# Kernel optimization log

Hardware: AMD Instinct MI355X
Metric: run time of the kernel (lower is better)

Reference implementation:

```python
import jax, jax.numpy as jnp
import numpy as np

E = 8192   # line-graph nodes (edges of g)
N = 4096   # graph nodes
FIN = 64   # in_feats
FOUT = 64  # out_feats
H = FOUT // 2
BN_EPS = 1e-5


def _linear_params(k, fan_in):
    kw, kb = jax.random.split(k)
    s = 1.0 / np.sqrt(fan_in)
    w = jax.random.uniform(kw, (H, fan_in), jnp.float32, -s, s)
    b = jax.random.uniform(kb, (H,), jnp.float32, -s, s)
    return w, b


def setup_inputs() -> dict:
    key = jax.random.key(0)
    ks = jax.random.split(key, 12)
    inp = {}
    inp["y"] = jax.random.normal(ks[0], (E, FIN), jnp.float32)
    inp["deg_g"] = jax.random.uniform(ks[1], (N,), jnp.float32)  # unused in forward
    inp["g_a1"] = jnp.zeros((N, N), jnp.float32)                  # unused in forward
    # adjacency-like 0/1 matrices, sparse pattern stored dense (as th.mm expects)
    inp["lg_a1"] = (jax.random.uniform(ks[2], (E, E)) < (8.0 / E)).astype(jnp.float32)
    inp["pm"] = (jax.random.uniform(ks[3], (N, E)) < (2.0 / N)).astype(jnp.float32)
    inp["pd"] = (jax.random.uniform(ks[4], (N, E)) < (2.0 / N)).astype(jnp.float32)
    inp["theta_y_w"], inp["theta_y_b"] = _linear_params(ks[5], FIN)
    inp["theta_y_r_w"], inp["theta_y_r_b"] = _linear_params(ks[6], FIN)
    inp["gamma_a_w"], inp["gamma_a_b"] = _linear_params(ks[7], FIN)
    inp["gamma_x_w"], inp["gamma_x_b"] = _linear_params(ks[8], FOUT)
    inp["gamma_a_r_w"], inp["gamma_a_r_b"] = _linear_params(ks[9], FIN)
    inp["gamma_x_r_w"], inp["gamma_x_r_b"] = _linear_params(ks[10], FOUT)
    inp["bn_x_w"] = jnp.ones((FOUT,), jnp.float32)
    inp["bn_x_b"] = jnp.zeros((FOUT,), jnp.float32)
    inp["bn_y_w"] = jnp.ones((FOUT,), jnp.float32)
    inp["bn_y_b"] = jnp.zeros((FOUT,), jnp.float32)
    return inp


def _bn(x, w, b):
    # BatchNorm2d on [B, C, 1, 1] in training mode == per-channel batch norm
    # with biased variance over the row (batch) dimension.
    m = x.mean(0)
    v = jnp.mean((x - m) ** 2, axis=0)
    return (x - m) * jax.lax.rsqrt(v + BN_EPS) * w + b


def reference(y, deg_g, g_a1, lg_a1, pm, pd,
              theta_y_w, theta_y_b, theta_y_r_w, theta_y_r_b,
              gamma_a_w, gamma_a_b, gamma_x_w, gamma_x_b,
              gamma_a_r_w, gamma_a_r_b, gamma_x_r_w, gamma_x_r_b,
              bn_x_w, bn_x_b, bn_y_w, bn_y_b):
    pd_y = pd @ y                                        # [N, FIN]
    x_r = pd_y @ theta_y_r_w.T + theta_y_r_b             # [N, H]
    x = pd_y @ theta_y_w.T + theta_y_b                   # [N, H]
    x = jnp.concatenate([x, jax.nn.relu(x_r)], axis=1)   # [N, FOUT]
    x = _bn(x, bn_x_w, bn_x_b)
    pm_x = pm.T @ x                                      # [E, FOUT]
    lg_y = lg_a1 @ y                                     # [E, FIN] (computed once; torch computes it twice, same math)
    y_r = (lg_y @ gamma_a_r_w.T + gamma_a_r_b) + (pm_x @ gamma_x_r_w.T + gamma_x_r_b)
    y_n = (lg_y @ gamma_a_w.T + gamma_a_b) + (pm_x @ gamma_x_w.T + gamma_x_b)
    y_out = jnp.concatenate([y_n, jax.nn.relu(y_r)], axis=1)  # [E, FOUT]
    return _bn(y_out, bn_y_w, bn_y_b)
```

## Files before the change

kernel.cpp:

```cpp
#include <hip/hip_runtime.h>

typedef unsigned int uint_t;
typedef unsigned short ushort_t;
typedef unsigned long long ull_t;
typedef uint_t nvec4 __attribute__((ext_vector_type(4)));

#define SLOTS 48

__device__ __forceinline__ float bcast(float v, int k) {
    union { float f; int i; } x; x.f = v;
    int r = __builtin_amdgcn_readlane(x.i, k);
    union { int i; float f; } y2; y2.i = r;
    return y2.f;
}

__global__ __launch_bounds__(256) void stream_gather_kernel(
    const float* __restrict__ lg, const float* __restrict__ pd,
    const float* __restrict__ pm, const float* __restrict__ y,
    float* __restrict__ lg_y, float* __restrict__ pd_y,
    ushort_t* __restrict__ pm_keys, uint_t* __restrict__ pm_counts)
{
    __shared__ ushort_t sIdx[4][SLOTS];
    const int lane = threadIdx.x & 63;
    const int wv = threadIdx.x >> 6;
    const int wid = blockIdx.x * 4 + wv;
    const float* A;
    int row;
    if (wid < 8192)       { row = wid;         A = lg; }
    else if (wid < 12288) { row = wid - 8192;  A = pd; }
    else                  { row = wid - 12288; A = pm; }

    const nvec4* ap = (const nvec4*)(A + (size_t)row * 8192);
    ushort_t* slice = sIdx[wv];
    const ull_t lt = (1ull << lane) - 1ull;

    nvec4 buf[16];
    #pragma unroll
    for (int i = 0; i < 16; ++i)
        buf[i] = __builtin_nontemporal_load(ap + i * 64 + lane);

    uint_t cnt = 0;
    #pragma unroll
    for (int pp = 0; pp < 32; pp += 16) {
        #pragma unroll
        for (int i = 0; i < 16; ++i) {
            nvec4 c = buf[i];
            if (pp == 0)
                buf[i] = __builtin_nontemporal_load(ap + (16 + i) * 64 + lane);
            uint_t a0 = c.x, a1 = c.y, a2 = c.z, a3 = c.w;
            ull_t m = __ballot((a0 | a1 | a2 | a3) != 0u);
            if (m) {
                ull_t m0 = __ballot(a0 != 0u);
                ull_t m1 = __ballot(a1 != 0u);
                ull_t m2 = __ballot(a2 != 0u);
                ull_t m3 = __ballot(a3 != 0u);
                uint_t c0 = (uint_t)__popcll(m0), c1 = (uint_t)__popcll(m1);
                uint_t c2 = (uint_t)__popcll(m2);
                uint_t o0 = cnt + (uint_t)__popcll(m0 & lt);
                uint_t o1 = cnt + c0 + (uint_t)__popcll(m1 & lt);
                uint_t o2 = cnt + c0 + c1 + (uint_t)__popcll(m2 & lt);
                uint_t o3 = cnt + c0 + c1 + c2 + (uint_t)__popcll(m3 & lt);
                int j = (pp + i) * 256 + lane * 4;
                if (a0 && o0 < SLOTS) slice[o0] = (ushort_t)(j + 0);
                if (a1 && o1 < SLOTS) slice[o1] = (ushort_t)(j + 1);
                if (a2 && o2 < SLOTS) slice[o2] = (ushort_t)(j + 2);
                if (a3 && o3 < SLOTS) slice[o3] = (ushort_t)(j + 3);
                cnt += (uint_t)(__popcll(m0) + __popcll(m1) +
                                __popcll(m2) + __popcll(m3));
            }
        }
    }
    if (cnt > SLOTS) cnt = SLOTS;

    if (wid >= 12288) {
        if (lane == 0) pm_counts[row] = cnt;
        if (lane < (int)cnt) pm_keys[(size_t)row * SLOTS + lane] = slice[lane];
        return;
    }
    float a0 = 0.f, a1 = 0.f, a2 = 0.f, a3 = 0.f;
    uint_t i = 0;
    for (; i + 4 <= cnt; i += 4) {
        int j0 = slice[i + 0], j1 = slice[i + 1];
        int j2 = slice[i + 2], j3 = slice[i + 3];
        a0 += y[(size_t)j0 * 64 + lane];
        a1 += y[(size_t)j1 * 64 + lane];
        a2 += y[(size_t)j2 * 64 + lane];
        a3 += y[(size_t)j3 * 64 + lane];
    }
    for (; i < cnt; ++i) a0 += y[(size_t)slice[i] * 64 + lane];
    float acc = (a0 + a1) + (a2 + a3);
    if (wid < 8192) lg_y[(size_t)row * 64 + lane] = acc;
    else            pd_y[(size_t)row * 64 + lane] = acc;
}

__global__ __launch_bounds__(256) void xlin_kernel(
    const float* __restrict__ pd_y,
    const float* __restrict__ wt, const float* __restrict__ bt,
    const float* __restrict__ wr, const float* __restrict__ br,
    float* __restrict__ x_raw, float* __restrict__ stats_x)
{
    __shared__ float red[2][4][64];
    const int wave = threadIdx.x >> 6, lane = threadIdx.x & 63;
    const float* wsrc = (lane < 32) ? (wt + lane * 64) : (wr + (lane - 32) * 64);
    float wreg[64];
    const float4* wp = (const float4*)wsrc;
    #pragma unroll
    for (int q = 0; q < 16; ++q) {
        float4 t = wp[q];
        wreg[q * 4 + 0] = t.x; wreg[q * 4 + 1] = t.y;
        wreg[q * 4 + 2] = t.z; wreg[q * 4 + 3] = t.w;
    }
    float bias = (lane < 32) ? bt[lane] : br[lane - 32];
    float s1 = 0.f, s2 = 0.f;
    const int row0 = (blockIdx.x * 4 + wave) * 8;
    for (int r = 0; r < 8; ++r) {
        int row = row0 + r;
        float xv = pd_y[(size_t)row * 64 + lane];
        float acc = bias;
        #pragma unroll
        for (int k = 0; k < 64; ++k) acc = fmaf(bcast(xv, k), wreg[k], acc);
        if (lane >= 32) acc = fmaxf(acc, 0.f);
        x_raw[(size_t)row * 64 + lane] = acc;
        s1 += acc; s2 += acc * acc;
    }
    red[0][wave][lane] = s1; red[1][wave][lane] = s2;
    __syncthreads();
    if (wave == 0) {
        float a = 0.f, b = 0.f;
        #pragma unroll
        for (int w = 0; w < 4; ++w) { a += red[0][w][lane]; b += red[1][w][lane]; }
        atomicAdd(&stats_x[lane], a);
        atomicAdd(&stats_x[64 + lane], b);
    }
}

__global__ __launch_bounds__(256) void scatter_kernel(
    const ushort_t* __restrict__ pm_keys, const uint_t* __restrict__ pm_counts,
    const float* __restrict__ x_raw, const float* __restrict__ stats_x,
    const float* __restrict__ bnxw, const float* __restrict__ bnxb,
    float* __restrict__ pm_x)
{
    const int lane = threadIdx.x & 63;
    const int row = blockIdx.x * 4 + (threadIdx.x >> 6);
    float mean = stats_x[lane] * (1.f / 4096.f);
    float var  = fmaxf(stats_x[64 + lane] * (1.f / 4096.f) - mean * mean, 0.f);
    float rstd = rsqrtf(var + 1e-5f);
    float scale = rstd * bnxw[lane];
    float shift = bnxb[lane] - mean * scale;
    const ushort_t* slice = pm_keys + (size_t)row * SLOTS;
    uint_t cnt = pm_counts[row];
    float xb = fmaf(x_raw[(size_t)row * 64 + lane], scale, shift);
    for (uint_t i = 0; i < cnt; ++i) {
        int e = slice[i];
        atomicAdd(&pm_x[(size_t)e * 64 + lane], xb);
    }
}

__global__ __launch_bounds__(256) void ylin_kernel(
    const float* __restrict__ lg_y, const float* __restrict__ pm_x,
    const float* __restrict__ wa, const float* __restrict__ ba,
    const float* __restrict__ wx, const float* __restrict__ bx,
    const float* __restrict__ war, const float* __restrict__ bar,
    const float* __restrict__ wxr, const float* __restrict__ bxr,
    float* __restrict__ yraw, float* __restrict__ stats_y)
{
    __shared__ float red[2][4][64];
    const int wave = threadIdx.x >> 6, lane = threadIdx.x & 63;
    const float* s1p = (lane < 32) ? (wa + lane * 64) : (war + (lane - 32) * 64);
    const float* s2p = (lane < 32) ? (wx + lane * 64) : (wxr + (lane - 32) * 64);
    float w1[64], w2[64];
    {
        const float4* p1 = (const float4*)s1p;
        const float4* p2 = (const float4*)s2p;
        #pragma unroll
        for (int q = 0; q < 16; ++q) {
            float4 t1 = p1[q], t2 = p2[q];
            w1[q * 4 + 0] = t1.x; w1[q * 4 + 1] = t1.y;
            w1[q * 4 + 2] = t1.z; w1[q * 4 + 3] = t1.w;
            w2[q * 4 + 0] = t2.x; w2[q * 4 + 1] = t2.y;
            w2[q * 4 + 2] = t2.z; w2[q * 4 + 3] = t2.w;
        }
    }
    float bias = (lane < 32) ? (ba[lane] + bx[lane])
                             : (bar[lane - 32] + bxr[lane - 32]);
    float s1 = 0.f, s2 = 0.f;
    const int row0 = (blockIdx.x * 4 + wave) * 8;
    for (int r = 0; r < 8; ++r) {
        int row = row0 + r;
        float lv = lg_y[(size_t)row * 64 + lane];
        float pv = pm_x[(size_t)row * 64 + lane];
        float acc = bias;
        #pragma unroll
        for (int k = 0; k < 64; ++k) {
            acc = fmaf(bcast(lv, k), w1[k], acc);
            acc = fmaf(bcast(pv, k), w2[k], acc);
        }
        if (lane >= 32) acc = fmaxf(acc, 0.f);
        yraw[(size_t)row * 64 + lane] = acc;
        s1 += acc; s2 += acc * acc;
    }
    red[0][wave][lane] = s1; red[1][wave][lane] = s2;
    __syncthreads();
    if (wave == 0) {
        float a = 0.f, b = 0.f;
        #pragma unroll
        for (int w = 0; w < 4; ++w) { a += red[0][w][lane]; b += red[1][w][lane]; }
        atomicAdd(&stats_y[lane], a);
        atomicAdd(&stats_y[64 + lane], b);
    }
}

__global__ __launch_bounds__(256) void bny_kernel(
    float* __restrict__ yraw, const float* __restrict__ stats_y,
    const float* __restrict__ bnyw, const float* __restrict__ bnyb)
{
    int idx = blockIdx.x * 256 + threadIdx.x;
    int c = idx & 63;
    float mean = stats_y[c] * (1.f / 8192.f);
    float var  = fmaxf(stats_y[64 + c] * (1.f / 8192.f) - mean * mean, 0.f);
    float rstd = rsqrtf(var + 1e-5f);
    yraw[idx] = (yraw[idx] - mean) * rstd * bnyw[c] + bnyb[c];
}

extern "C" void kernel_launch(void* const* d_in, const int* in_sizes, int n_in,
                              void* d_out, int out_size, void* d_ws, size_t ws_size,
                              hipStream_t stream)
{
    const float* y     = (const float*)d_in[0];
    const float* lg_a1 = (const float*)d_in[3];
    const float* pm    = (const float*)d_in[4];
    const float* pd    = (const float*)d_in[5];
    const float* th_w  = (const float*)d_in[6];
    const float* th_b  = (const float*)d_in[7];
    const float* thr_w = (const float*)d_in[8];
    const float* thr_b = (const float*)d_in[9];
    const float* ga_w  = (const float*)d_in[10];
    const float* ga_b  = (const float*)d_in[11];
    const float* gx_w  = (const float*)d_in[12];
    const float* gx_b  = (const float*)d_in[13];
    const float* gar_w = (const float*)d_in[14];
    const float* gar_b = (const float*)d_in[15];
    const float* gxr_w = (const float*)d_in[16];
    const float* gxr_b = (const float*)d_in[17];
    const float* bnx_w = (const float*)d_in[18];
    const float* bnx_b = (const float*)d_in[19];
    const float* bny_w = (const float*)d_in[20];
    const float* bny_b = (const float*)d_in[21];

    char* ws = (char*)d_ws;
    float* stats_x = (float*)ws;
    float* stats_y = (float*)(ws + 1024);
    float* pm_x    = (float*)(ws + 2048);
    const size_t zero_bytes = 2048 + (size_t)8192 * 64 * 4;
    float* pd_y  = (float*)(ws + zero_bytes);
    float* lg_y  = pd_y + (size_t)4096 * 64;
    float* x_raw = lg_y + (size_t)8192 * 64;
    ushort_t* pm_keys = (ushort_t*)(x_raw + (size_t)4096 * 64);
    uint_t* pm_counts = (uint_t*)(pm_keys + (size_t)4096 * SLOTS);
    float* yraw  = (float*)d_out;

    (void)hipMemsetAsync(d_ws, 0, zero_bytes, stream);

    stream_gather_kernel<<<4096, 256, 0, stream>>>(lg_a1, pd, pm, y,
                                                   lg_y, pd_y,
                                                   pm_keys, pm_counts);
    xlin_kernel<<<128, 256, 0, stream>>>(pd_y, th_w, th_b, thr_w, thr_b,
                                         x_raw, stats_x);
    scatter_kernel<<<1024, 256, 0, stream>>>(pm_keys, pm_counts, x_raw, stats_x,
                                             bnx_w, bnx_b, pm_x);
    ylin_kernel<<<256, 256, 0, stream>>>(lg_y, pm_x, ga_w, ga_b, gx_w, gx_b,
                                         gar_w, gar_b, gxr_w, gxr_b,
                                         yraw, stats_y);
    bny_kernel<<<2048, 256, 0, stream>>>(yraw, stats_y, bny_w, bny_b);
}
```

Baseline: 574.5 us.

## Split dense streaming into a chunk-interleaved bitmask pass plus separate gather

```diff
diff --git a/kernel.cpp b/kernel.cpp
--- a/kernel.cpp
+++ b/kernel.cpp
@@ -6,6 +6,12 @@
 typedef uint_t nvec4 __attribute__((ext_vector_type(4)));
 
 #define SLOTS 48
+
+#define LG_CHUNK_END 262144
+#define PD_CHUNK_END 393216
+#define TOT_CHUNKS   524288
+#define STREAM_WAVES 8192
+#define CHUNK_ITERS  (TOT_CHUNKS / STREAM_WAVES)
 
 __device__ __forceinline__ float bcast(float v, int k) {
     union { float f; int i; } x; x.f = v;
@@ -14,9 +20,51 @@
     return y2.f;
 }
 
-__global__ __launch_bounds__(256) void stream_gather_kernel(
+__device__ __forceinline__ const nvec4* chunk_ptr(int c, const float* lg,
+                                                  const float* pd, const float* pm) {
+    if (c < LG_CHUNK_END) return (const nvec4*)(lg + (size_t)c * 256);
+    if (c < PD_CHUNK_END) return (const nvec4*)(pd + (size_t)(c - LG_CHUNK_END) * 256);
+    return (const nvec4*)(pm + (size_t)(c - PD_CHUNK_END) * 256);
+}
+
+__global__ __launch_bounds__(256) void mask_stream_kernel(
     const float* __restrict__ lg, const float* __restrict__ pd,
-    const float* __restrict__ pm, const float* __restrict__ y,
+    const float* __restrict__ pm, ull_t* __restrict__ maskbuf)
+{
+    const int lane = threadIdx.x & 63;
+    const int w = blockIdx.x * 4 + (threadIdx.x >> 6);
+
+    #pragma unroll
+    for (int g = 0; g < CHUNK_ITERS / 4; ++g) {
+        nvec4 b[4];
+        #pragma unroll
+        for (int k = 0; k < 4; ++k) {
+            int c = (g * 4 + k) * STREAM_WAVES + w;
+            b[k] = __builtin_nontemporal_load(chunk_ptr(c, lg, pd, pm) + lane);
+        }
+        #pragma unroll
+        for (int k = 0; k < 4; ++k) {
+            int c = (g * 4 + k) * STREAM_WAVES + w;
+            nvec4 v = b[k];
+            ull_t m0 = 0, m1 = 0, m2 = 0, m3 = 0;
+            ull_t any = __ballot((v.x | v.y | v.z | v.w) != 0u);
+            if (any) {
+                m0 = __ballot(v.x != 0u);
+                m1 = __ballot(v.y != 0u);
+                m2 = __ballot(v.z != 0u);
+                m3 = __ballot(v.w != 0u);
+            }
+            if (lane < 4) {
+                ull_t out = (lane & 2) ? ((lane & 1) ? m3 : m2)
+                                       : ((lane & 1) ? m1 : m0);
+                maskbuf[(size_t)c * 4 + lane] = out;
+            }
+        }
+    }
+}
+
+__global__ __launch_bounds__(256) void gather2_kernel(
+    const ull_t* __restrict__ maskbuf, const float* __restrict__ y,
     float* __restrict__ lg_y, float* __restrict__ pd_y,
     ushort_t* __restrict__ pm_keys, uint_t* __restrict__ pm_counts)
 {
@@ -24,55 +72,52 @@
     const int lane = threadIdx.x & 63;
     const int wv = threadIdx.x >> 6;
     const int wid = blockIdx.x * 4 + wv;
-    const float* A;
-    int row;
-    if (wid < 8192)       { row = wid;         A = lg; }
-    else if (wid < 12288) { row = wid - 8192;  A = pd; }
-    else                  { row = wid - 12288; A = pm; }
-
-    const nvec4* ap = (const nvec4*)(A + (size_t)row * 8192);
+    int row, kind;
+    size_t cbase;
+    if (wid < 8192)       { row = wid;         kind = 0; cbase = (size_t)row * 32; }
+    else if (wid < 12288) { row = wid - 8192;  kind = 1; cbase = LG_CHUNK_END + (size_t)row * 32; }
+    else                  { row = wid - 12288; kind = 2; cbase = PD_CHUNK_END + (size_t)row * 32; }
+
+    const ulonglong2* mp = (const ulonglong2*)(maskbuf + cbase * 4);
+    ulonglong2 t = mp[lane];
+    ull_t u0 = t.x, u1 = t.y;
+    uint_t c = (uint_t)(__popcll(u0) + __popcll(u1));
+
+    uint_t inc = c;
+    #pragma unroll
+    for (int d = 1; d < 64; d <<= 1) {
+        uint_t tt = __shfl_up(inc, d, 64);
+        if (lane >= d) inc += tt;
+    }
+    uint_t off = inc - c;
+    uint_t tot = __shfl(inc, 63, 64);
+
     ushort_t* slice = sIdx[wv];
-    const ull_t lt = (1ull << lane) - 1ull;
-
-    nvec4 buf[16];
-    #pragma unroll
-    for (int i = 0; i < 16; ++i)
-        buf[i] = __builtin_nontemporal_load(ap + i * 64 + lane);
-
-    uint_t cnt = 0;
-    #pragma unroll
-    for (int pp = 0; pp < 32; pp += 16) {
-        #pragma unroll
-        for (int i = 0; i < 16; ++i) {
-            nvec4 c = buf[i];
-            if (pp == 0)
-                buf[i] = __builtin_nontemporal_load(ap + (16 + i) * 64 + lane);
-            uint_t a0 = c.x, a1 = c.y, a2 = c.z, a3 = c.w;
-            ull_t m = __ballot((a0 | a1 | a2 | a3) != 0u);
-            if (m) {
-                ull_t m0 = __ballot(a0 != 0u);
-                ull_t m1 = __ballot(a1 != 0u);
-                ull_t m2 = __ballot(a2 != 0u);
-                ull_t m3 = __ballot(a3 != 0u);
-                uint_t c0 = (uint_t)__popcll(m0), c1 = (uint_t)__popcll(m1);
-                uint_t c2 = (uint_t)__popcll(m2);
-                uint_t o0 = cnt + (uint_t)__popcll(m0 & lt);
-                uint_t o1 = cnt + c0 + (uint_t)__popcll(m1 & lt);
-                uint_t o2 = cnt + c0 + c1 + (uint_t)__popcll(m2 & lt);
-                uint_t o3 = cnt + c0 + c1 + c2 + (uint_t)__popcll(m3 & lt);
-                int j = (pp + i) * 256 + lane * 4;
-                if (a0 && o0 < SLOTS) slice[o0] = (ushort_t)(j + 0);
-                if (a1 && o1 < SLOTS) slice[o1] = (ushort_t)(j + 1);
-                if (a2 && o2 < SLOTS) slice[o2] = (ushort_t)(j + 2);
-                if (a3 && o3 < SLOTS) slice[o3] = (ushort_t)(j + 3);
-                cnt += (uint_t)(__popcll(m0) + __popcll(m1) +
-                                __popcll(m2) + __popcll(m3));
-            }
-        }
-    }
-    if (cnt > SLOTS) cnt = SLOTS;
-
-    if (wid >= 12288) {
+    {
+        int ui = 2 * lane;
+        int basecol = (ui >> 2) * 256 + (ui & 3);
+        ull_t u = u0;
+        while (u) {
+            int b = __builtin_ctzll(u);
+            u &= u - 1;
+            if (off < SLOTS) slice[off] = (ushort_t)(basecol + b * 4);
+            ++off;
+        }
+    }
+    {
+        int ui = 2 * lane + 1;
+        int basecol = (ui >> 2) * 256 + (ui & 3);
+        ull_t u = u1;
+        while (u) {
+            int b = __builtin_ctzll(u);
+            u &= u - 1;
+            if (off < SLOTS) slice[off] = (ushort_t)(basecol + b * 4);
+            ++off;
+        }
+    }
+    uint_t cnt = (tot > SLOTS) ? SLOTS : tot;
+
+    if (kind == 2) {
         if (lane == 0) pm_counts[row] = cnt;
         if (lane < (int)cnt) pm_keys[(size_t)row * SLOTS + lane] = slice[lane];
         return;
@@ -89,8 +134,8 @@
     }
     for (; i < cnt; ++i) a0 += y[(size_t)slice[i] * 64 + lane];
     float acc = (a0 + a1) + (a2 + a3);
-    if (wid < 8192) lg_y[(size_t)row * 64 + lane] = acc;
-    else            pd_y[(size_t)row * 64 + lane] = acc;
+    if (kind == 0) lg_y[(size_t)row * 64 + lane] = acc;
+    else           pd_y[(size_t)row * 64 + lane] = acc;
 }
 
 __global__ __launch_bounds__(256) void xlin_kernel(
@@ -257,13 +302,15 @@
     float* x_raw = lg_y + (size_t)8192 * 64;
     ushort_t* pm_keys = (ushort_t*)(x_raw + (size_t)4096 * 64);
     uint_t* pm_counts = (uint_t*)(pm_keys + (size_t)4096 * SLOTS);
+    size_t moff = ((size_t)((char*)(pm_counts + 4096) - ws) + 1023) & ~(size_t)1023;
+    ull_t* maskbuf = (ull_t*)(ws + moff);
     float* yraw  = (float*)d_out;
 
     (void)hipMemsetAsync(d_ws, 0, zero_bytes, stream);
 
-    stream_gather_kernel<<<4096, 256, 0, stream>>>(lg_a1, pd, pm, y,
-                                                   lg_y, pd_y,
-                                                   pm_keys, pm_counts);
+    mask_stream_kernel<<<2048, 256, 0, stream>>>(lg_a1, pd, pm, maskbuf);
+    gather2_kernel<<<4096, 256, 0, stream>>>(maskbuf, y, lg_y, pd_y,
+                                             pm_keys, pm_counts);
     xlin_kernel<<<128, 256, 0, stream>>>(pd_y, th_w, th_b, thr_w, thr_b,
                                          x_raw, stats_x);
     scatter_kernel<<<1024, 256, 0, stream>>>(pm_keys, pm_counts, x_raw, stats_x,
```

Result: slower. 603.9 us (+5.1%).

## Stream dense rows through LDS with async global_load_lds ring buffer

Applied to the files above, without the earlier changes.

```diff
diff --git a/kernel.cpp b/kernel.cpp
--- a/kernel.cpp
+++ b/kernel.cpp
@@ -14,12 +14,59 @@
     return y2.f;
 }
 
+__device__ __forceinline__ void compact_chunk(nvec4 c, int cc, int lane, ull_t lt,
+                                              uint_t& cnt, ushort_t* slice)
+{
+    uint_t a0 = c.x, a1 = c.y, a2 = c.z, a3 = c.w;
+    ull_t m = __ballot((a0 | a1 | a2 | a3) != 0u);
+    if (m) {
+        ull_t m0 = __ballot(a0 != 0u);
+        ull_t m1 = __ballot(a1 != 0u);
+        ull_t m2 = __ballot(a2 != 0u);
+        ull_t m3 = __ballot(a3 != 0u);
+        uint_t c0 = (uint_t)__popcll(m0), c1 = (uint_t)__popcll(m1);
+        uint_t c2 = (uint_t)__popcll(m2);
+        uint_t o0 = cnt + (uint_t)__popcll(m0 & lt);
+        uint_t o1 = cnt + c0 + (uint_t)__popcll(m1 & lt);
+        uint_t o2 = cnt + c0 + c1 + (uint_t)__popcll(m2 & lt);
+        uint_t o3 = cnt + c0 + c1 + c2 + (uint_t)__popcll(m3 & lt);
+        int j = cc * 256 + lane * 4;
+        if (a0 && o0 < SLOTS) slice[o0] = (ushort_t)(j + 0);
+        if (a1 && o1 < SLOTS) slice[o1] = (ushort_t)(j + 1);
+        if (a2 && o2 < SLOTS) slice[o2] = (ushort_t)(j + 2);
+        if (a3 && o3 < SLOTS) slice[o3] = (ushort_t)(j + 3);
+        cnt += (uint_t)(__popcll(m0) + __popcll(m1) +
+                        __popcll(m2) + __popcll(m3));
+    }
+}
+
+__device__ __forceinline__ void gld_lds16(const void* g, void* l) {
+    __builtin_amdgcn_global_load_lds(
+        (const __attribute__((address_space(1))) void*)g,
+        (__attribute__((address_space(3))) void*)l, 16, 0, 0);
+}
+
+#define VMWAIT(n) asm volatile("s_waitcnt vmcnt(" #n ")" ::: "memory")
+#define LKWAIT(v) asm volatile("s_waitcnt lgkmcnt(0)" : "+v"(v) :: "memory")
+
+#define STEP(c, wn)                                                          \
+    {                                                                        \
+        VMWAIT(wn);                                                          \
+        nvec4 v = ((const nvec4*)&sbuf[wv][(c) & 7][0])[lane];               \
+        LKWAIT(v);                                                           \
+        if ((c) + 8 < 32)                                                    \
+            gld_lds16(rowb + ((c) + 8) * 1024 + (size_t)lane * 16,           \
+                      &sbuf[wv][(c) & 7][0]);                                \
+        compact_chunk(v, (c), lane, lt, cnt, slice);                         \
+    }
+
 __global__ __launch_bounds__(256) void stream_gather_kernel(
     const float* __restrict__ lg, const float* __restrict__ pd,
     const float* __restrict__ pm, const float* __restrict__ y,
     float* __restrict__ lg_y, float* __restrict__ pd_y,
     ushort_t* __restrict__ pm_keys, uint_t* __restrict__ pm_counts)
 {
+    __shared__ float sbuf[4][8][256];
     __shared__ ushort_t sIdx[4][SLOTS];
     const int lane = threadIdx.x & 63;
     const int wv = threadIdx.x >> 6;
@@ -30,46 +77,29 @@
     else if (wid < 12288) { row = wid - 8192;  A = pd; }
     else                  { row = wid - 12288; A = pm; }
 
-    const nvec4* ap = (const nvec4*)(A + (size_t)row * 8192);
     ushort_t* slice = sIdx[wv];
     const ull_t lt = (1ull << lane) - 1ull;
-
-    nvec4 buf[16];
-    #pragma unroll
-    for (int i = 0; i < 16; ++i)
-        buf[i] = __builtin_nontemporal_load(ap + i * 64 + lane);
+    const char* rowb = (const char*)(A + (size_t)row * 8192);
+
+    gld_lds16(rowb + 0 * 1024 + (size_t)lane * 16, &sbuf[wv][0][0]);
+    gld_lds16(rowb + 1 * 1024 + (size_t)lane * 16, &sbuf[wv][1][0]);
+    gld_lds16(rowb + 2 * 1024 + (size_t)lane * 16, &sbuf[wv][2][0]);
+    gld_lds16(rowb + 3 * 1024 + (size_t)lane * 16, &sbuf[wv][3][0]);
+    gld_lds16(rowb + 4 * 1024 + (size_t)lane * 16, &sbuf[wv][4][0]);
+    gld_lds16(rowb + 5 * 1024 + (size_t)lane * 16, &sbuf[wv][5][0]);
+    gld_lds16(rowb + 6 * 1024 + (size_t)lane * 16, &sbuf[wv][6][0]);
+    gld_lds16(rowb + 7 * 1024 + (size_t)lane * 16, &sbuf[wv][7][0]);
 
     uint_t cnt = 0;
-    #pragma unroll
-    for (int pp = 0; pp < 32; pp += 16) {
-        #pragma unroll
-        for (int i = 0; i < 16; ++i) {
-            nvec4 c = buf[i];
-            if (pp == 0)
-                buf[i] = __builtin_nontemporal_load(ap + (16 + i) * 64 + lane);
-            uint_t a0 = c.x, a1 = c.y, a2 = c.z, a3 = c.w;
-            ull_t m = __ballot((a0 | a1 | a2 | a3) != 0u);
-            if (m) {
-                ull_t m0 = __ballot(a0 != 0u);
-                ull_t m1 = __ballot(a1 != 0u);
-                ull_t m2 = __ballot(a2 != 0u);
-                ull_t m3 = __ballot(a3 != 0u);
-                uint_t c0 = (uint_t)__popcll(m0), c1 = (uint_t)__popcll(m1);
-                uint_t c2 = (uint_t)__popcll(m2);
-                uint_t o0 = cnt + (uint_t)__popcll(m0 & lt);
-                uint_t o1 = cnt + c0 + (uint_t)__popcll(m1 & lt);
-                uint_t o2 = cnt + c0 + c1 + (uint_t)__popcll(m2 & lt);
-                uint_t o3 = cnt + c0 + c1 + c2 + (uint_t)__popcll(m3 & lt);
-                int j = (pp + i) * 256 + lane * 4;
-                if (a0 && o0 < SLOTS) slice[o0] = (ushort_t)(j + 0);
-                if (a1 && o1 < SLOTS) slice[o1] = (ushort_t)(j + 1);
-                if (a2 && o2 < SLOTS) slice[o2] = (ushort_t)(j + 2);
-                if (a3 && o3 < SLOTS) slice[o3] = (ushort_t)(j + 3);
-                cnt += (uint_t)(__popcll(m0) + __popcll(m1) +
-                                __popcll(m2) + __popcll(m3));
-            }
-        }
-    }
+    STEP(0, 7);  STEP(1, 7);  STEP(2, 7);  STEP(3, 7);
+    STEP(4, 7);  STEP(5, 7);  STEP(6, 7);  STEP(7, 7);
+    STEP(8, 7);  STEP(9, 7);  STEP(10, 7); STEP(11, 7);
+    STEP(12, 7); STEP(13, 7); STEP(14, 7); STEP(15, 7);
+    STEP(16, 7); STEP(17, 7); STEP(18, 7); STEP(19, 7);
+    STEP(20, 7); STEP(21, 7); STEP(22, 7); STEP(23, 7);
+    STEP(24, 7); STEP(25, 6); STEP(26, 5); STEP(27, 4);
+    STEP(28, 3); STEP(29, 2); STEP(30, 1); STEP(31, 0);
+
     if (cnt > SLOTS) cnt = SLOTS;
 
     if (wid >= 12288) {
```

After: 596.8 us. +3.9%, slower.

## Fuse post-gather stages into one persistent kernel with grid barriers

Applied to the files above, without the earlier changes.

```diff
diff --git a/kernel.cpp b/kernel.cpp
--- a/kernel.cpp
+++ b/kernel.cpp
@@ -93,34 +93,67 @@
     else            pd_y[(size_t)row * 64 + lane] = acc;
 }
 
-__global__ __launch_bounds__(256) void xlin_kernel(
-    const float* __restrict__ pd_y,
+__device__ __forceinline__ void gbar(uint_t* cnt, uint_t target) {
+    __threadfence();
+    __syncthreads();
+    if (threadIdx.x == 0) {
+        __hip_atomic_fetch_add(cnt, 1u, __ATOMIC_RELEASE,
+                               __HIP_MEMORY_SCOPE_AGENT);
+        while (__hip_atomic_load(cnt, __ATOMIC_ACQUIRE,
+                                 __HIP_MEMORY_SCOPE_AGENT) < target)
+            __builtin_amdgcn_s_sleep(2);
+    }
+    __syncthreads();
+}
+
+__device__ __forceinline__ float agload(const float* p) {
+    return __hip_atomic_load(p, __ATOMIC_RELAXED, __HIP_MEMORY_SCOPE_AGENT);
+}
+
+__global__ __launch_bounds__(256) void tail_kernel(
+    const float* __restrict__ pd_y, const float* __restrict__ lg_y,
+    const ushort_t* __restrict__ pm_keys, const uint_t* __restrict__ pm_counts,
     const float* __restrict__ wt, const float* __restrict__ bt,
     const float* __restrict__ wr, const float* __restrict__ br,
-    float* __restrict__ x_raw, float* __restrict__ stats_x)
+    const float* __restrict__ bnxw, const float* __restrict__ bnxb,
+    const float* __restrict__ wa, const float* __restrict__ ba,
+    const float* __restrict__ wx, const float* __restrict__ bx,
+    const float* __restrict__ war, const float* __restrict__ bar,
+    const float* __restrict__ wxr, const float* __restrict__ bxr,
+    const float* __restrict__ bnyw, const float* __restrict__ bnyb,
+    float* __restrict__ pm_x, float* __restrict__ stats_x,
+    float* __restrict__ stats_y, uint_t* __restrict__ bar_cnt,
+    float* __restrict__ yraw)
 {
     __shared__ float red[2][4][64];
     const int wave = threadIdx.x >> 6, lane = threadIdx.x & 63;
-    const float* wsrc = (lane < 32) ? (wt + lane * 64) : (wr + (lane - 32) * 64);
+    const int gwave = blockIdx.x * 4 + wave;
+    const uint_t nblk = gridDim.x;
+
     float wreg[64];
-    const float4* wp = (const float4*)wsrc;
+    {
+        const float* wsrc = (lane < 32) ? (wt + lane * 64)
+                                        : (wr + (lane - 32) * 64);
+        const float4* wp = (const float4*)wsrc;
+        #pragma unroll
+        for (int q = 0; q < 16; ++q) {
+            float4 t = wp[q];
+            wreg[q * 4 + 0] = t.x; wreg[q * 4 + 1] = t.y;
+            wreg[q * 4 + 2] = t.z; wreg[q * 4 + 3] = t.w;
+        }
+    }
+    float biasx = (lane < 32) ? bt[lane] : br[lane - 32];
+    float xr[4];
+    float s1 = 0.f, s2 = 0.f;
+    const int xrow0 = gwave * 4;
     #pragma unroll
-    for (int q = 0; q < 16; ++q) {
-        float4 t = wp[q];
-        wreg[q * 4 + 0] = t.x; wreg[q * 4 + 1] = t.y;
-        wreg[q * 4 + 2] = t.z; wreg[q * 4 + 3] = t.w;
-    }
-    float bias = (lane < 32) ? bt[lane] : br[lane - 32];
-    float s1 = 0.f, s2 = 0.f;
-    const int row0 = (blockIdx.x * 4 + wave) * 8;
-    for (int r = 0; r < 8; ++r) {
-        int row = row0 + r;
-        float xv = pd_y[(size_t)row * 64 + lane];
-        float acc = bias;
+    for (int r = 0; r < 4; ++r) {
+        float xv = pd_y[(size_t)(xrow0 + r) * 64 + lane];
+        float acc = biasx;
         #pragma unroll
         for (int k = 0; k < 64; ++k) acc = fmaf(bcast(xv, k), wreg[k], acc);
         if (lane >= 32) acc = fmaxf(acc, 0.f);
-        x_raw[(size_t)row * 64 + lane] = acc;
+        xr[r] = acc;
         s1 += acc; s2 += acc * acc;
     }
     red[0][wave][lane] = s1; red[1][wave][lane] = s2;
@@ -132,71 +165,65 @@
         atomicAdd(&stats_x[lane], a);
         atomicAdd(&stats_x[64 + lane], b);
     }
-}
-
-__global__ __launch_bounds__(256) void scatter_kernel(
-    const ushort_t* __restrict__ pm_keys, const uint_t* __restrict__ pm_counts,
-    const float* __restrict__ x_raw, const float* __restrict__ stats_x,
-    const float* __restrict__ bnxw, const float* __restrict__ bnxb,
-    float* __restrict__ pm_x)
-{
-    const int lane = threadIdx.x & 63;
-    const int row = blockIdx.x * 4 + (threadIdx.x >> 6);
-    float mean = stats_x[lane] * (1.f / 4096.f);
-    float var  = fmaxf(stats_x[64 + lane] * (1.f / 4096.f) - mean * mean, 0.f);
-    float rstd = rsqrtf(var + 1e-5f);
-    float scale = rstd * bnxw[lane];
-    float shift = bnxb[lane] - mean * scale;
-    const ushort_t* slice = pm_keys + (size_t)row * SLOTS;
-    uint_t cnt = pm_counts[row];
-    float xb = fmaf(x_raw[(size_t)row * 64 + lane], scale, shift);
-    for (uint_t i = 0; i < cnt; ++i) {
-        int e = slice[i];
-        atomicAdd(&pm_x[(size_t)e * 64 + lane], xb);
-    }
-}
-
-__global__ __launch_bounds__(256) void ylin_kernel(
-    const float* __restrict__ lg_y, const float* __restrict__ pm_x,
-    const float* __restrict__ wa, const float* __restrict__ ba,
-    const float* __restrict__ wx, const float* __restrict__ bx,
-    const float* __restrict__ war, const float* __restrict__ bar,
-    const float* __restrict__ wxr, const float* __restrict__ bxr,
-    float* __restrict__ yraw, float* __restrict__ stats_y)
-{
-    __shared__ float red[2][4][64];
-    const int wave = threadIdx.x >> 6, lane = threadIdx.x & 63;
-    const float* s1p = (lane < 32) ? (wa + lane * 64) : (war + (lane - 32) * 64);
-    const float* s2p = (lane < 32) ? (wx + lane * 64) : (wxr + (lane - 32) * 64);
-    float w1[64], w2[64];
+    gbar(&bar_cnt[0], nblk);
+
     {
+        float s = agload(&stats_x[lane]);
+        float q = agload(&stats_x[64 + lane]);
+        float mean = s * (1.f / 4096.f);
+        float var  = fmaxf(q * (1.f / 4096.f) - mean * mean, 0.f);
+        float rstd = rsqrtf(var + 1e-5f);
+        float scale = rstd * bnxw[lane];
+        float shift = bnxb[lane] - mean * scale;
+        #pragma unroll
+        for (int r = 0; r < 4; ++r) {
+            int row = xrow0 + r;
+            uint_t cnt = pm_counts[row];
+            const ushort_t* slice = pm_keys + (size_t)row * SLOTS;
+            float xb = fmaf(xr[r], scale, shift);
+            for (uint_t i = 0; i < cnt; ++i) {
+                int e = slice[i];
+                atomicAdd(&pm_x[(size_t)e * 64 + lane], xb);
+            }
+        }
+    }
+    gbar(&bar_cnt[1], nblk);
+
+    float w2r[64];
+    {
+        const float* s1p = (lane < 32) ? (wa + lane * 64)
+                                       : (war + (lane - 32) * 64);
+        const float* s2p = (lane < 32) ? (wx + lane * 64)
+                                       : (wxr + (lane - 32) * 64);
         const float4* p1 = (const float4*)s1p;
         const float4* p2 = (const float4*)s2p;
         #pragma unroll
         for (int q = 0; q < 16; ++q) {
             float4 t1 = p1[q], t2 = p2[q];
-            w1[q * 4 + 0] = t1.x; w1[q * 4 + 1] = t1.y;
-            w1[q * 4 + 2] = t1.z; w1[q * 4 + 3] = t1.w;
-            w2[q * 4 + 0] = t2.x; w2[q * 4 + 1] = t2.y;
-            w2[q * 4 + 2] = t2.z; w2[q * 4 + 3] = t2.w;
-        }
-    }
-    float bias = (lane < 32) ? (ba[lane] + bx[lane])
-                             : (bar[lane - 32] + bxr[lane - 32]);
-    float s1 = 0.f, s2 = 0.f;
-    const int row0 = (blockIdx.x * 4 + wave) * 8;
+            wreg[q * 4 + 0] = t1.x; wreg[q * 4 + 1] = t1.y;
+            wreg[q * 4 + 2] = t1.z; wreg[q * 4 + 3] = t1.w;
+            w2r[q * 4 + 0] = t2.x; w2r[q * 4 + 1] = t2.y;
+            w2r[q * 4 + 2] = t2.z; w2r[q * 4 + 3] = t2.w;
+        }
+    }
+    float biasy = (lane < 32) ? (ba[lane] + bx[lane])
+                              : (bar[lane - 32] + bxr[lane - 32]);
+    float yv[8];
+    s1 = 0.f; s2 = 0.f;
+    const int yrow0 = gwave * 8;
+    #pragma unroll
     for (int r = 0; r < 8; ++r) {
-        int row = row0 + r;
+        int row = yrow0 + r;
         float lv = lg_y[(size_t)row * 64 + lane];
-        float pv = pm_x[(size_t)row * 64 + lane];
-        float acc = bias;
+        float pv = agload(&pm_x[(size_t)row * 64 + lane]);
+        float acc = biasy;
         #pragma unroll
         for (int k = 0; k < 64; ++k) {
-            acc = fmaf(bcast(lv, k), w1[k], acc);
-            acc = fmaf(bcast(pv, k), w2[k], acc);
+            acc = fmaf(bcast(lv, k), wreg[k], acc);
+            acc = fmaf(bcast(pv, k), w2r[k], acc);
         }
         if (lane >= 32) acc = fmaxf(acc, 0.f);
-        yraw[(size_t)row * 64 + lane] = acc;
+        yv[r] = acc;
         s1 += acc; s2 += acc * acc;
     }
     red[0][wave][lane] = s1; red[1][wave][lane] = s2;
@@ -208,18 +235,20 @@
         atomicAdd(&stats_y[lane], a);
         atomicAdd(&stats_y[64 + lane], b);
     }
-}
-
-__global__ __launch_bounds__(256) void bny_kernel(
-    float* __restrict__ yraw, const float* __restrict__ stats_y,
-    const float* __restrict__ bnyw, const float* __restrict__ bnyb)
-{
-    int idx = blockIdx.x * 256 + threadIdx.x;
-    int c = idx & 63;
-    float mean = stats_y[c] * (1.f / 8192.f);
-    float var  = fmaxf(stats_y[64 + c] * (1.f / 8192.f) - mean * mean, 0.f);
-    float rstd = rsqrtf(var + 1e-5f);
-    yraw[idx] = (yraw[idx] - mean) * rstd * bnyw[c] + bnyb[c];
+    gbar(&bar_cnt[2], nblk);
+
+    {
+        float s = agload(&stats_y[lane]);
+        float q = agload(&stats_y[64 + lane]);
+        float mean = s * (1.f / 8192.f);
+        float var  = fmaxf(q * (1.f / 8192.f) - mean * mean, 0.f);
+        float rstd = rsqrtf(var + 1e-5f);
+        float sc = rstd * bnyw[lane];
+        float sh = bnyb[lane] - mean * sc;
+        #pragma unroll
+        for (int r = 0; r < 8; ++r)
+            yraw[(size_t)(yrow0 + r) * 64 + lane] = fmaf(yv[r], sc, sh);
+    }
 }
 
 extern "C" void kernel_launch(void* const* d_in, const int* in_sizes, int n_in,
@@ -250,12 +279,12 @@
     char* ws = (char*)d_ws;
     float* stats_x = (float*)ws;
     float* stats_y = (float*)(ws + 1024);
+    uint_t* bar_cnt = (uint_t*)(ws + 1536);
     float* pm_x    = (float*)(ws + 2048);
     const size_t zero_bytes = 2048 + (size_t)8192 * 64 * 4;
     float* pd_y  = (float*)(ws + zero_bytes);
     float* lg_y  = pd_y + (size_t)4096 * 64;
-    float* x_raw = lg_y + (size_t)8192 * 64;
-    ushort_t* pm_keys = (ushort_t*)(x_raw + (size_t)4096 * 64);
+    ushort_t* pm_keys = (ushort_t*)(lg_y + (size_t)8192 * 64);
     uint_t* pm_counts = (uint_t*)(pm_keys + (size_t)4096 * SLOTS);
     float* yraw  = (float*)d_out;
 
@@ -264,12 +293,12 @@
     stream_gather_kernel<<<4096, 256, 0, stream>>>(lg_a1, pd, pm, y,
                                                    lg_y, pd_y,
                                                    pm_keys, pm_counts);
-    xlin_kernel<<<128, 256, 0, stream>>>(pd_y, th_w, th_b, thr_w, thr_b,
-                                         x_raw, stats_x);
-    scatter_kernel<<<1024, 256, 0, stream>>>(pm_keys, pm_counts, x_raw, stats_x,
-                                             bnx_w, bnx_b, pm_x);
-    ylin_kernel<<<256, 256, 0, stream>>>(lg_y, pm_x, ga_w, ga_b, gx_w, gx_b,
+    tail_kernel<<<256, 256, 0, stream>>>(pd_y, lg_y, pm_keys, pm_counts,
+                                         th_w, th_b, thr_w, thr_b,
+                                         bnx_w, bnx_b,
+                                         ga_w, ga_b, gx_w, gx_b,
                                          gar_w, gar_b, gxr_w, gxr_b,
-                                         yraw, stats_y);
-    bny_kernel<<<2048, 256, 0, stream>>>(yraw, stats_y, bny_w, bny_b);
-}
+                                         bny_w, bny_b,
+                                         pm_x, stats_x, stats_y, bar_cnt,
+                                         yraw);
+}
```

Result: slower. 659.6 us (+14.8%).
